# Kernel optimization log

Hardware: AMD Instinct MI355X
Metric: run time of the kernel (lower is better)

The kernel has to match this reference:

```python
import jax, jax.numpy as jnp
import numpy as np

H = 12
D_MODEL = 768
D_K = D_MODEL // H  # 64


def setup_inputs() -> dict:
    key = jax.random.key(0)
    ks = jax.random.split(key, 16)
    B, S, D = 4, 1024, D_MODEL
    scale = 1.0 / np.sqrt(D)
    inp = {
        "query": jax.random.normal(ks[0], (B, S, D), jnp.float32),
        "key": jax.random.normal(ks[1], (B, S, D), jnp.float32),
        "value": jax.random.normal(ks[2], (B, S, D), jnp.float32),
        "times": jax.random.normal(ks[3], (2, B, S, D), jnp.float32),
        # learned params (Linear weights stored torch-style [out, in])
        "Wq": jax.random.normal(ks[4], (D, D), jnp.float32) * scale,
        "bq": jnp.zeros((D,), jnp.float32),
        "Wk": jax.random.normal(ks[5], (D, D), jnp.float32) * scale,
        "bk": jnp.zeros((D,), jnp.float32),
        "Wv": jax.random.normal(ks[6], (D, D), jnp.float32) * scale,
        "bv": jnp.zeros((D,), jnp.float32),
        "Wt": jax.random.normal(ks[7], (D, D), jnp.float32) * scale,
        "bt": jnp.zeros((D,), jnp.float32),
        "Wo": jax.random.normal(ks[8], (D, D), jnp.float32) * scale,
        "bo": jnp.zeros((D,), jnp.float32),
    }
    return inp


def _split_heads(x, B, S):
    # [B,S,D] -> [B,H,S,D_K]
    return x.reshape(B, S, H, D_K).transpose(0, 2, 1, 3)


def reference(query, key, value, times, Wq, bq, Wk, bk, Wv, bv, Wt, bt, Wo, bo):
    B, S, D = query.shape
    inv_sqrt_dk = 1.0 / jnp.sqrt(jnp.asarray(D_K, query.dtype))
    # q/k/v projections are identical across time-loop iterations; hoist them.
    q = _split_heads(query @ Wq.T + bq, B, S)   # [B,H,S,dk]
    k = _split_heads(key @ Wk.T + bk, B, S)
    v = _split_heads(value @ Wv.T + bv, B, S)
    x = jnp.zeros_like(q)
    n_times = times.shape[0]
    for i in range(n_times):  # small fixed loop over time embeddings
        t = _split_heads(times[i] @ Wt.T + bt, B, S)
        # dual-score attention: query.time + query.key, each scaled by 1/sqrt(d_k)
        scores = (jnp.einsum('bhqd,bhkd->bhqk', q, t)
                  + jnp.einsum('bhqd,bhkd->bhqk', q, k)) * inv_sqrt_dk
        p = jax.nn.softmax(scores, axis=-1)
        x = x + jnp.einsum('bhqk,bhkd->bhqd', p, v)
    x = x.transpose(0, 2, 1, 3).reshape(B, S, H * D_K)
    return x @ Wo.T + bo
```

## Files before the change

kernel.cpp:

```cpp
#include <hip/hip_runtime.h>
#include <hip/hip_fp16.h>

typedef _Float16 v8h __attribute__((ext_vector_type(8)));
typedef _Float16 v4h __attribute__((ext_vector_type(4)));
typedef float v4f __attribute__((ext_vector_type(4)));

#define MFMA_F16 __builtin_amdgcn_mfma_f32_16x16x32_f16
#define MFMA16_F16 __builtin_amdgcn_mfma_f32_16x16x16f16
#define EXP2F __builtin_amdgcn_exp2f

__device__ static inline void async_copy16(const void* g, void* l) {
  __builtin_amdgcn_global_load_lds(
      (const __attribute__((address_space(1))) void*)g,
      (__attribute__((address_space(3))) void*)l, 16, 0, 0);
}

struct CastArgs {
  const float* src[10];
  _Float16* dst[10];
  int start[11];
  float scale[10];
};
__global__ void cast_all(CastArgs a) {
  const int g = blockIdx.x * 256 + threadIdx.x;
  if (g >= a.start[10]) return;
  int z = 0;
  #pragma unroll
  for (int i = 1; i < 10; ++i) if (g >= a.start[i]) z = i;
  const int i0 = g - a.start[z];
  const float sc = a.scale[z];
  const float* s = a.src[z] + (size_t)i0 * 8;
  const float4 f0 = *(const float4*)s;
  const float4 f1 = *(const float4*)(s + 4);
  v8h o = {(_Float16)(f0.x * sc), (_Float16)(f0.y * sc),
           (_Float16)(f0.z * sc), (_Float16)(f0.w * sc),
           (_Float16)(f1.x * sc), (_Float16)(f1.y * sc),
           (_Float16)(f1.z * sc), (_Float16)(f1.w * sc)};
  *(v8h*)(a.dst[z] + (size_t)i0 * 8) = o;
}

struct GemmArgs {
  const _Float16* A1[4]; const _Float16* A2[4];
  const _Float16* W1[4]; const _Float16* W2[4];
  const float* b1[4];    const float* b2[4];
  void* out[4];
  float bscale[4];
  int K[4];
  int mode[4];
};

template <int MT>
__global__ __launch_bounds__(256) void gemm_mt(GemmArgs g) {
  constexpr int iA = MT / 32;
  constexpr int NMT = MT / 32;
  __shared__ _Float16 a_lds[MT * 64];
  __shared__ _Float16 w_lds[128 * 64];
  const int z = blockIdx.z;
  const int KK = g.K[z];
  const int tid = threadIdx.x;
  const int w = tid >> 6, lane = tid & 63, quad = lane >> 4, l16 = lane & 15;
  const int m0 = blockIdx.x * MT, n0 = blockIdx.y * 128;
  const int wm = (w >> 1) * (MT / 2), wn = (w & 1) * 64;

  size_t srcOff[4]; int ldsOff[4];
  #pragma unroll
  for (int i = 0; i < 4; ++i) {
    const int c = i * 256 + tid, row = c >> 3, slot = c & 7;
    srcOff[i] = (size_t)row * 768 + (size_t)((slot ^ (row & 7)) * 8);
    ldsOff[i] = (i * 256 + w * 64) * 8;
  }

  v4f acc[NMT][4] = {};

  for (int k0 = 0; k0 < KK; k0 += 64) {
    const _Float16* Asrc = (k0 < 768) ? g.A1[z] : g.A2[z];
    const _Float16* Wsrc = (k0 < 768) ? g.W1[z] : g.W2[z];
    const int kc = (k0 < 768) ? k0 : k0 - 768;
    __syncthreads();
    #pragma unroll
    for (int i = 0; i < 4; ++i) {
      if (i < iA)
        async_copy16(Asrc + (size_t)m0 * 768 + kc + srcOff[i], &a_lds[ldsOff[i]]);
      async_copy16(Wsrc + (size_t)n0 * 768 + kc + srcOff[i], &w_lds[ldsOff[i]]);
    }
    __syncthreads();

    #pragma unroll
    for (int kh = 0; kh < 2; ++kh) {
      v8h af[NMT], bf[4];
      #pragma unroll
      for (int mt = 0; mt < NMT; ++mt) {
        const int r = wm + mt * 16 + l16;
        af[mt] = *(const v8h*)&a_lds[r * 64 + (((kh * 4 + quad) ^ (r & 7)) * 8)];
      }
      #pragma unroll
      for (int nt = 0; nt < 4; ++nt) {
        const int r = wn + nt * 16 + l16;
        bf[nt] = *(const v8h*)&w_lds[r * 64 + (((kh * 4 + quad) ^ (r & 7)) * 8)];
      }
      #pragma unroll
      for (int mt = 0; mt < NMT; ++mt)
        #pragma unroll
        for (int nt = 0; nt < 4; ++nt)
          acc[mt][nt] = MFMA_F16(af[mt], bf[nt], acc[mt][nt], 0, 0, 0);
    }
  }

  const int mode = g.mode[z];
  #pragma unroll
  for (int nt = 0; nt < 4; ++nt) {
    const int col = n0 + wn + nt * 16 + l16;
    float bv = g.b1[z][col] * g.bscale[z];
    if (g.b2[z]) bv += g.b2[z][col];
    if (mode == 1) {
      _Float16* outp = (_Float16*)g.out[z];
      const int h = col >> 6, dk = col & 63;
      #pragma unroll
      for (int mt = 0; mt < NMT; ++mt) {
        const int row = m0 + wm + mt * 16 + quad * 4;
        const int b = row >> 10, s = row & 1023;
        const int sp = (s & ~31) | ((s & 12) << 1) | ((s & 16) >> 2);
        v4h pack = {(_Float16)(acc[mt][nt][0] + bv), (_Float16)(acc[mt][nt][1] + bv),
                    (_Float16)(acc[mt][nt][2] + bv), (_Float16)(acc[mt][nt][3] + bv)};
        *(v4h*)&outp[(size_t)((b * 12 + h) * 64 + dk) * 1024 + sp] = pack;
      }
    } else {
      #pragma unroll
      for (int mt = 0; mt < NMT; ++mt)
        #pragma unroll
        for (int r = 0; r < 4; ++r) {
          const int row = m0 + wm + mt * 16 + quad * 4 + r;
          const float v = acc[mt][nt][r] + bv;
          if (mode == 2) ((float*)g.out[z])[(size_t)row * 768 + col] = v;
          else ((_Float16*)g.out[z])[(size_t)row * 768 + col] = (_Float16)v;
        }
    }
  }
}

__global__ __launch_bounds__(256) void attn(
    const _Float16* __restrict__ Q,
    const _Float16* __restrict__ KT0, const _Float16* __restrict__ KT1,
    const _Float16* __restrict__ Vt,
    _Float16* __restrict__ X)
{
  __shared__ _Float16 kt0[2][64 * 64];
  __shared__ _Float16 kt1[2][64 * 64];
  __shared__ _Float16 vt[2][64 * 64];

  const int tid = threadIdx.x;
  const int w = tid >> 6, lane = tid & 63, quad = lane >> 4, l16 = lane & 15;
  const int bh = blockIdx.y, b = bh / 12, h = bh % 12;
  const int q0 = blockIdx.x * 64;
  const size_t base = (size_t)b * 1024 * 768 + h * 64;

  const _Float16* KT0b = KT0 + base;
  const _Float16* KT1b = KT1 + base;
  const _Float16* Vtb = Vt + (size_t)bh * 64 * 1024;

  size_t ktOff[2], vOff[2]; int ldsOff[2];
  #pragma unroll
  for (int i = 0; i < 2; ++i) {
    const int c = i * 256 + w * 64 + lane, row = c >> 3, slot = c & 7;
    const int logical = slot ^ (row & 7);
    ktOff[i] = (size_t)row * 768 + (size_t)(logical * 8);
    vOff[i] = (size_t)row * 1024 + (size_t)(logical * 8);
    ldsOff[i] = c * 8;
  }
  auto stage = [&](int kv0, int buf) {
    #pragma unroll
    for (int i = 0; i < 2; ++i) {
      async_copy16(KT0b + (size_t)kv0 * 768 + ktOff[i], &kt0[buf][ldsOff[i]]);
      async_copy16(KT1b + (size_t)kv0 * 768 + ktOff[i], &kt1[buf][ldsOff[i]]);
      async_copy16(Vtb + (size_t)kv0 + vOff[i], &vt[buf][ldsOff[i]]);
    }
  };

  const _Float16* Qw = Q + base + (size_t)(q0 + w * 16) * 768;
  const v8h qf0 = *(const v8h*)(Qw + (size_t)l16 * 768 + quad * 8);
  const v8h qf1 = *(const v8h*)(Qw + (size_t)l16 * 768 + 32 + quad * 8);

  const _Float16 one = (_Float16)1.f;
  const v4h ones = {one, one, one, one};
  v4f o[2][4] = {};
  v4f osum[2] = {};

  stage(0, 0);
  for (int cc = 0; cc < 16; ++cc) {
    __syncthreads();
    if (cc < 15) stage((cc + 1) * 64, (cc + 1) & 1);
    const _Float16* k0p = &kt0[cc & 1][0];
    const _Float16* k1p = &kt1[cc & 1][0];
    const _Float16* vp = &vt[cc & 1][0];

    v4f s[2][4];
    #pragma unroll
    for (int kvt = 0; kvt < 4; ++kvt) {
      const int r = kvt * 16 + l16, rw = r & 7;
      const v8h k00 = *(const v8h*)&k0p[r * 64 + ((quad ^ rw) * 8)];
      const v8h k01 = *(const v8h*)&k0p[r * 64 + (((4 + quad) ^ rw) * 8)];
      const v8h k10 = *(const v8h*)&k1p[r * 64 + ((quad ^ rw) * 8)];
      const v8h k11 = *(const v8h*)&k1p[r * 64 + (((4 + quad) ^ rw) * 8)];
      s[0][kvt] = MFMA_F16(k00, qf0, v4f{}, 0, 0, 0);
      s[0][kvt] = MFMA_F16(k01, qf1, s[0][kvt], 0, 0, 0);
      s[1][kvt] = MFMA_F16(k10, qf0, v4f{}, 0, 0, 0);
      s[1][kvt] = MFMA_F16(k11, qf1, s[1][kvt], 0, 0, 0);
    }

    v4h pb[2][4];
    #pragma unroll
    for (int t = 0; t < 2; ++t)
      #pragma unroll
      for (int kvt = 0; kvt < 4; ++kvt) {
        pb[t][kvt] = v4h{(_Float16)EXP2F(s[t][kvt][0]),
                         (_Float16)EXP2F(s[t][kvt][1]),
                         (_Float16)EXP2F(s[t][kvt][2]),
                         (_Float16)EXP2F(s[t][kvt][3])};
        osum[t] = MFMA16_F16(ones, pb[t][kvt], osum[t], 0, 0, 0);
      }

    #pragma unroll
    for (int dkt = 0; dkt < 4; ++dkt) {
      const int row = dkt * 16 + l16, rw = row & 7;
      #pragma unroll
      for (int gph = 0; gph < 2; ++gph) {
        const int phys = (gph * 4 + quad) ^ rw;
        const v8h vv = *(const v8h*)&vp[row * 64 + phys * 8];
        const v4h lo = {vv[0], vv[1], vv[2], vv[3]};
        const v4h hi = {vv[4], vv[5], vv[6], vv[7]};
        #pragma unroll
        for (int t = 0; t < 2; ++t) {
          o[t][dkt] = MFMA16_F16(lo, pb[t][gph * 2], o[t][dkt], 0, 0, 0);
          o[t][dkt] = MFMA16_F16(hi, pb[t][gph * 2 + 1], o[t][dkt], 0, 0, 0);
        }
      }
    }
  }

  const float i0 = 1.0f / osum[0][0], i1 = 1.0f / osum[1][0];

  _Float16* Xw = X + base + (size_t)(q0 + w * 16 + l16) * 768;
  #pragma unroll
  for (int dkt = 0; dkt < 4; ++dkt) {
    v4h pack;
    #pragma unroll
    for (int r = 0; r < 4; ++r)
      pack[r] = (_Float16)(o[0][dkt][r] * i0 + o[1][dkt][r] * i1);
    *(v4h*)&Xw[dkt * 16 + quad * 4] = pack;
  }
}

extern "C" void kernel_launch(void* const* d_in, const int* in_sizes, int n_in,
                              void* d_out, int out_size, void* d_ws, size_t ws_size,
                              hipStream_t stream) {
  const float* query = (const float*)d_in[0];
  const float* key   = (const float*)d_in[1];
  const float* value = (const float*)d_in[2];
  const float* times = (const float*)d_in[3];
  const float* Wq = (const float*)d_in[4];  const float* bq = (const float*)d_in[5];
  const float* Wk = (const float*)d_in[6];  const float* bk = (const float*)d_in[7];
  const float* Wv = (const float*)d_in[8];  const float* bv = (const float*)d_in[9];
  const float* Wt = (const float*)d_in[10]; const float* bt = (const float*)d_in[11];
  const float* Wo = (const float*)d_in[12]; const float* bo = (const float*)d_in[13];
  float* out = (float*)d_out;

  const size_t NELEM = (size_t)4096 * 768;
  const size_t WELEM = (size_t)768 * 768;
  const float QSCALE = 0.125f * 1.4426950408889634f;

  char* ws = (char*)d_ws;
  size_t off = 0;
  auto alloc = [&](size_t bytes) {
    void* p = ws + off; off += (bytes + 255) & ~(size_t)255; return p;
  };
  _Float16* qh  = (_Float16*)alloc(NELEM * 2);
  _Float16* kh  = (_Float16*)alloc(NELEM * 2);
  _Float16* vh  = (_Float16*)alloc(NELEM * 2);
  _Float16* wqh = (_Float16*)alloc(WELEM * 2);
  _Float16* wkh = (_Float16*)alloc(WELEM * 2);
  _Float16* wvh = (_Float16*)alloc(WELEM * 2);
  _Float16* wth = (_Float16*)alloc(WELEM * 2);
  _Float16* woh = (_Float16*)alloc(WELEM * 2);
  _Float16* Qh  = (_Float16*)alloc(NELEM * 2);
  _Float16* KT0 = (_Float16*)alloc(NELEM * 2);
  _Float16* KT1 = (_Float16*)alloc(NELEM * 2);
  _Float16* Vt  = (_Float16*)alloc(NELEM * 2);
  _Float16* t0h = (_Float16*)d_out;
  _Float16* t1h = t0h + NELEM;
  _Float16* Xh = qh;

  CastArgs ca = {};
  const int nA8 = (int)(NELEM / 8), nW8 = (int)(WELEM / 8);
  const float* csrc[10] = {query, key, value, times, times + NELEM, Wq, Wk, Wv, Wt, Wo};
  _Float16* cdst[10] = {qh, kh, vh, t0h, t1h, wqh, wkh, wvh, wth, woh};
  int acc8 = 0;
  for (int i = 0; i < 10; ++i) {
    ca.src[i] = csrc[i]; ca.dst[i] = cdst[i];
    ca.start[i] = acc8;
    acc8 += (i < 5) ? nA8 : nW8;
    ca.scale[i] = (i == 5) ? QSCALE : 1.0f;
  }
  ca.start[10] = acc8;
  cast_all<<<dim3((acc8 + 255) / 256), 256, 0, stream>>>(ca);

  GemmArgs pa = {};
  pa.A1[0] = t0h; pa.A2[0] = kh; pa.W1[0] = wth; pa.W2[0] = wkh;
  pa.b1[0] = bt; pa.b2[0] = bk; pa.out[0] = KT0; pa.bscale[0] = 1.0f;
  pa.K[0] = 1536; pa.mode[0] = 0;
  pa.A1[1] = t1h; pa.A2[1] = kh; pa.W1[1] = wth; pa.W2[1] = wkh;
  pa.b1[1] = bt; pa.b2[1] = bk; pa.out[1] = KT1; pa.bscale[1] = 1.0f;
  pa.K[1] = 1536; pa.mode[1] = 0;
  pa.A1[2] = qh; pa.A2[2] = qh; pa.W1[2] = wqh; pa.W2[2] = wqh;
  pa.b1[2] = bq; pa.b2[2] = nullptr; pa.out[2] = Qh; pa.bscale[2] = QSCALE;
  pa.K[2] = 768; pa.mode[2] = 0;
  pa.A1[3] = vh; pa.A2[3] = vh; pa.W1[3] = wvh; pa.W2[3] = wvh;
  pa.b1[3] = bv; pa.b2[3] = nullptr; pa.out[3] = Vt; pa.bscale[3] = 1.0f;
  pa.K[3] = 768; pa.mode[3] = 1;
  gemm_mt<128><<<dim3(32, 6, 4), 256, 0, stream>>>(pa);

  attn<<<dim3(16, 48), 256, 0, stream>>>(Qh, KT0, KT1, Vt, Xh);

  GemmArgs oa = {};
  oa.A1[0] = Xh; oa.A2[0] = Xh; oa.W1[0] = woh; oa.W2[0] = woh;
  oa.b1[0] = bo; oa.b2[0] = nullptr; oa.out[0] = out; oa.bscale[0] = 1.0f;
  oa.K[0] = 768; oa.mode[0] = 2;
  gemm_mt<64><<<dim3(64, 6, 1), 256, 0, stream>>>(oa);
}
```

Baseline: 237.2 us.

## Compute second time-key as difference projection to halve its GEMM K dimension

```diff
diff --git a/kernel.cpp b/kernel.cpp
--- a/kernel.cpp
+++ b/kernel.cpp
@@ -17,6 +17,7 @@
 
 struct CastArgs {
   const float* src[10];
+  const float* src2;
   _Float16* dst[10];
   int start[11];
   float scale[10];
@@ -28,10 +29,17 @@
   #pragma unroll
   for (int i = 1; i < 10; ++i) if (g >= a.start[i]) z = i;
   const int i0 = g - a.start[z];
+  const float* s = a.src[z] + (size_t)i0 * 8;
+  float4 f0 = *(const float4*)s;
+  float4 f1 = *(const float4*)(s + 4);
+  if (z == 4) {
+    const float* s2 = a.src2 + (size_t)i0 * 8;
+    const float4 g0 = *(const float4*)s2;
+    const float4 g1 = *(const float4*)(s2 + 4);
+    f0 = make_float4(g0.x - f0.x, g0.y - f0.y, g0.z - f0.z, g0.w - f0.w);
+    f1 = make_float4(g1.x - f1.x, g1.y - f1.y, g1.z - f1.z, g1.w - f1.w);
+  }
   const float sc = a.scale[z];
-  const float* s = a.src[z] + (size_t)i0 * 8;
-  const float4 f0 = *(const float4*)s;
-  const float4 f1 = *(const float4*)(s + 4);
   v8h o = {(_Float16)(f0.x * sc), (_Float16)(f0.y * sc),
            (_Float16)(f0.z * sc), (_Float16)(f0.w * sc),
            (_Float16)(f1.x * sc), (_Float16)(f1.y * sc),
@@ -140,12 +148,12 @@
 
 __global__ __launch_bounds__(256) void attn(
     const _Float16* __restrict__ Q,
-    const _Float16* __restrict__ KT0, const _Float16* __restrict__ KT1,
+    const _Float16* __restrict__ KT0, const _Float16* __restrict__ D,
     const _Float16* __restrict__ Vt,
     _Float16* __restrict__ X)
 {
-  __shared__ _Float16 kt0[2][64 * 64];
-  __shared__ _Float16 kt1[2][64 * 64];
+  __shared__ _Float16 ktl[2][64 * 64];
+  __shared__ _Float16 dl[2][64 * 64];
   __shared__ _Float16 vt[2][64 * 64];
 
   const int tid = threadIdx.x;
@@ -154,8 +162,8 @@
   const int q0 = blockIdx.x * 64;
   const size_t base = (size_t)b * 1024 * 768 + h * 64;
 
-  const _Float16* KT0b = KT0 + base;
-  const _Float16* KT1b = KT1 + base;
+  const _Float16* KTb = KT0 + base;
+  const _Float16* Db = D + base;
   const _Float16* Vtb = Vt + (size_t)bh * 64 * 1024;
 
   size_t ktOff[2], vOff[2]; int ldsOff[2];
@@ -170,8 +178,8 @@
   auto stage = [&](int kv0, int buf) {
     #pragma unroll
     for (int i = 0; i < 2; ++i) {
-      async_copy16(KT0b + (size_t)kv0 * 768 + ktOff[i], &kt0[buf][ldsOff[i]]);
-      async_copy16(KT1b + (size_t)kv0 * 768 + ktOff[i], &kt1[buf][ldsOff[i]]);
+      async_copy16(KTb + (size_t)kv0 * 768 + ktOff[i], &ktl[buf][ldsOff[i]]);
+      async_copy16(Db + (size_t)kv0 * 768 + ktOff[i], &dl[buf][ldsOff[i]]);
       async_copy16(Vtb + (size_t)kv0 + vOff[i], &vt[buf][ldsOff[i]]);
     }
   };
@@ -189,8 +197,8 @@
   for (int cc = 0; cc < 16; ++cc) {
     __syncthreads();
     if (cc < 15) stage((cc + 1) * 64, (cc + 1) & 1);
-    const _Float16* k0p = &kt0[cc & 1][0];
-    const _Float16* k1p = &kt1[cc & 1][0];
+    const _Float16* k0p = &ktl[cc & 1][0];
+    const _Float16* dp = &dl[cc & 1][0];
     const _Float16* vp = &vt[cc & 1][0];
 
     v4f s[2][4];
@@ -199,12 +207,12 @@
       const int r = kvt * 16 + l16, rw = r & 7;
       const v8h k00 = *(const v8h*)&k0p[r * 64 + ((quad ^ rw) * 8)];
       const v8h k01 = *(const v8h*)&k0p[r * 64 + (((4 + quad) ^ rw) * 8)];
-      const v8h k10 = *(const v8h*)&k1p[r * 64 + ((quad ^ rw) * 8)];
-      const v8h k11 = *(const v8h*)&k1p[r * 64 + (((4 + quad) ^ rw) * 8)];
+      const v8h d0 = *(const v8h*)&dp[r * 64 + ((quad ^ rw) * 8)];
+      const v8h d1 = *(const v8h*)&dp[r * 64 + (((4 + quad) ^ rw) * 8)];
       s[0][kvt] = MFMA_F16(k00, qf0, v4f{}, 0, 0, 0);
       s[0][kvt] = MFMA_F16(k01, qf1, s[0][kvt], 0, 0, 0);
-      s[1][kvt] = MFMA_F16(k10, qf0, v4f{}, 0, 0, 0);
-      s[1][kvt] = MFMA_F16(k11, qf1, s[1][kvt], 0, 0, 0);
+      s[1][kvt] = MFMA_F16(d0, qf0, s[0][kvt], 0, 0, 0);
+      s[1][kvt] = MFMA_F16(d1, qf1, s[1][kvt], 0, 0, 0);
     }
 
     v4h pb[2][4];
@@ -283,16 +291,16 @@
   _Float16* woh = (_Float16*)alloc(WELEM * 2);
   _Float16* Qh  = (_Float16*)alloc(NELEM * 2);
   _Float16* KT0 = (_Float16*)alloc(NELEM * 2);
-  _Float16* KT1 = (_Float16*)alloc(NELEM * 2);
+  _Float16* Dh  = (_Float16*)alloc(NELEM * 2);
   _Float16* Vt  = (_Float16*)alloc(NELEM * 2);
   _Float16* t0h = (_Float16*)d_out;
-  _Float16* t1h = t0h + NELEM;
+  _Float16* difh = t0h + NELEM;
   _Float16* Xh = qh;
 
   CastArgs ca = {};
   const int nA8 = (int)(NELEM / 8), nW8 = (int)(WELEM / 8);
-  const float* csrc[10] = {query, key, value, times, times + NELEM, Wq, Wk, Wv, Wt, Wo};
-  _Float16* cdst[10] = {qh, kh, vh, t0h, t1h, wqh, wkh, wvh, wth, woh};
+  const float* csrc[10] = {query, key, value, times, times, Wq, Wk, Wv, Wt, Wo};
+  _Float16* cdst[10] = {qh, kh, vh, t0h, difh, wqh, wkh, wvh, wth, woh};
   int acc8 = 0;
   for (int i = 0; i < 10; ++i) {
     ca.src[i] = csrc[i]; ca.dst[i] = cdst[i];
@@ -301,15 +309,16 @@
     ca.scale[i] = (i == 5) ? QSCALE : 1.0f;
   }
   ca.start[10] = acc8;
+  ca.src2 = times + NELEM;
   cast_all<<<dim3((acc8 + 255) / 256), 256, 0, stream>>>(ca);
 
   GemmArgs pa = {};
   pa.A1[0] = t0h; pa.A2[0] = kh; pa.W1[0] = wth; pa.W2[0] = wkh;
   pa.b1[0] = bt; pa.b2[0] = bk; pa.out[0] = KT0; pa.bscale[0] = 1.0f;
   pa.K[0] = 1536; pa.mode[0] = 0;
-  pa.A1[1] = t1h; pa.A2[1] = kh; pa.W1[1] = wth; pa.W2[1] = wkh;
-  pa.b1[1] = bt; pa.b2[1] = bk; pa.out[1] = KT1; pa.bscale[1] = 1.0f;
-  pa.K[1] = 1536; pa.mode[1] = 0;
+  pa.A1[1] = difh; pa.A2[1] = difh; pa.W1[1] = wth; pa.W2[1] = wth;
+  pa.b1[1] = bt; pa.b2[1] = nullptr; pa.out[1] = Dh; pa.bscale[1] = 0.0f;
+  pa.K[1] = 768; pa.mode[1] = 0;
   pa.A1[2] = qh; pa.A2[2] = qh; pa.W1[2] = wqh; pa.W2[2] = wqh;
   pa.b1[2] = bq; pa.b2[2] = nullptr; pa.out[2] = Qh; pa.bscale[2] = QSCALE;
   pa.K[2] = 768; pa.mode[2] = 0;
@@ -318,7 +327,7 @@
   pa.K[3] = 768; pa.mode[3] = 1;
   gemm_mt<128><<<dim3(32, 6, 4), 256, 0, stream>>>(pa);
 
-  attn<<<dim3(16, 48), 256, 0, stream>>>(Qh, KT0, KT1, Vt, Xh);
+  attn<<<dim3(16, 48), 256, 0, stream>>>(Qh, KT0, Dh, Vt, Xh);
 
   GemmArgs oa = {};
   oa.A1[0] = Xh; oa.A2[0] = Xh; oa.W1[0] = woh; oa.W2[0] = woh;
```

Result: no change. 236.4 us (-0.3%).
